# Optimization experiments

Measured on AMD Instinct MI355X. Metric: run time of the kernel, lower is better.

## Reference

```python
import jax, jax.numpy as jnp
import numpy as np

EMBED_DIM = 1024
NUM_HEADS = 16
HEAD_DIM = EMBED_DIM // NUM_HEADS


def setup_inputs() -> dict:
    key = jax.random.key(0)
    ks = jax.random.split(key, 9)
    s = 1.0 / np.sqrt(EMBED_DIM)
    mk = lambda k: jax.random.uniform(k, (EMBED_DIM, EMBED_DIM), jnp.float32, -s, s)
    bk = lambda k: jax.random.uniform(k, (EMBED_DIM,), jnp.float32, -s, s)
    return {
        "input_tensor": jax.random.normal(ks[0], (4, 2048, EMBED_DIM), jnp.float32),
        "wq": mk(ks[1]), "bq": bk(ks[2]),
        "wk": mk(ks[3]), "bk_": bk(ks[4]),
        "wv": mk(ks[5]), "bv": bk(ks[6]),
        "wo": mk(ks[7]), "bo": bk(ks[8]),
    }


def reference(input_tensor, wq, bq, wk, bk_, wv, bv, wo, bo):
    B, S, E = input_tensor.shape
    H, D = NUM_HEADS, HEAD_DIM
    # torch Linear: y = x @ W.T + b
    q = input_tensor @ wq.T + bq
    k = input_tensor @ wk.T + bk_
    v = input_tensor @ wv.T + bv
    q = q.reshape(B, S, H, D).transpose(0, 2, 1, 3)  # [B,H,S,D]
    k = k.reshape(B, S, H, D).transpose(0, 2, 1, 3)
    v = v.reshape(B, S, H, D).transpose(0, 2, 1, 3)
    scores = jnp.einsum('bhsd,bhtd->bhst', q, k) / jnp.sqrt(jnp.float32(D))
    attn = jax.nn.softmax(scores, axis=-1)  # dropout p=0 -> identity
    out = jnp.einsum('bhst,bhtd->bhsd', attn, v)
    out = out.transpose(0, 2, 1, 3).reshape(B, S, E)
    return out @ wo.T + bo
```

## Files before the change

### kernel.cpp

```cpp
#include <hip/hip_runtime.h>

typedef __bf16 bf16x8 __attribute__((ext_vector_type(8)));
typedef float  f32x4  __attribute__((ext_vector_type(4)));
typedef float  f32x16 __attribute__((ext_vector_type(16)));
typedef unsigned u32x4 __attribute__((ext_vector_type(4)));

#define NB 4
#define SEQ 2048
#define EMB 1024
#define NH 16
#define HD 64
#define MTOT (NB * SEQ)

__device__ __forceinline__ unsigned short f2bf(float f) {
    unsigned u = __float_as_uint(f);
    return (unsigned short)((u + 0x7fffu + ((u >> 16) & 1u)) >> 16);
}

__device__ __forceinline__ void gload16(const void* g, void* l) {
    __builtin_amdgcn_global_load_lds(
        (const __attribute__((address_space(1))) unsigned int*)g,
        (__attribute__((address_space(3))) unsigned int*)l,
        16, 0, 0);
}

__global__ __launch_bounds__(256) void cast_f32_bf16(
    const float* __restrict__ src, unsigned short* __restrict__ dst, int n4) {
    int i = blockIdx.x * 256 + threadIdx.x;
    if (i < n4) {
        float4 v = ((const float4*)src)[i];
        ushort4 r;
        r.x = f2bf(v.x); r.y = f2bf(v.y); r.z = f2bf(v.z); r.w = f2bf(v.w);
        ((ushort4*)dst)[i] = r;
    }
}

__global__ __launch_bounds__(256) void cast4_f32_bf16(
    const float* __restrict__ a, const float* __restrict__ b,
    const float* __restrict__ c, const float* __restrict__ d,
    unsigned short* __restrict__ oa, unsigned short* __restrict__ ob,
    unsigned short* __restrict__ oc, unsigned short* __restrict__ od) {
    int which = blockIdx.x >> 10;
    int i = (blockIdx.x & 1023) * 256 + threadIdx.x;
    const float* src = which == 0 ? a : which == 1 ? b : which == 2 ? c : d;
    unsigned short* dst = which == 0 ? oa : which == 1 ? ob : which == 2 ? oc : od;
    float4 v = ((const float4*)src)[i];
    ushort4 r;
    r.x = f2bf(v.x); r.y = f2bf(v.y); r.z = f2bf(v.z); r.w = f2bf(v.w);
    ((ushort4*)dst)[i] = r;
}

template <int MODE>
__global__ __launch_bounds__(256) void gemm_bt(
    const unsigned short* __restrict__ A, const unsigned short* __restrict__ W,
    const float* __restrict__ bias, void* __restrict__ out, float oscale) {
    constexpr int K = EMB;
    __shared__ __align__(16) unsigned short As[128 * 64];
    __shared__ __align__(16) unsigned short Bs[128 * 64];

    const int lane = threadIdx.x & 63;
    const int wv   = threadIdx.x >> 6;
    const int wr   = wv >> 1, wc = wv & 1;
    const int m0   = blockIdx.y * 128, n0 = blockIdx.x * 128;

    f32x4 acc[4][4];
#pragma unroll
    for (int a = 0; a < 4; ++a)
#pragma unroll
        for (int b = 0; b < 4; ++b) acc[a][b] = (f32x4){0.f, 0.f, 0.f, 0.f};

    for (int kt = 0; kt < K / 64; ++kt) {
        if (kt) __syncthreads();
#pragma unroll
        for (int j = 0; j < 4; ++j) {
            int rb = (wv * 4 + j) * 8;
            int r  = rb + (lane >> 3);
            int c  = (lane & 7) * 8;
            gload16(A + (size_t)(m0 + r) * K + kt * 64 + c, &As[rb * 64]);
            gload16(W + (size_t)(n0 + r) * K + kt * 64 + c, &Bs[rb * 64]);
        }
        __syncthreads();
#pragma unroll
        for (int ks = 0; ks < 2; ++ks) {
            bf16x8 af[4], bf_[4];
#pragma unroll
            for (int x = 0; x < 4; ++x) {
                af[x]  = *(const bf16x8*)&As[(wr * 64 + x * 16 + (lane & 15)) * 64 + ks * 32 + (lane >> 4) * 8];
                bf_[x] = *(const bf16x8*)&Bs[(wc * 64 + x * 16 + (lane & 15)) * 64 + ks * 32 + (lane >> 4) * 8];
            }
#pragma unroll
            for (int mi = 0; mi < 4; ++mi)
#pragma unroll
                for (int ni = 0; ni < 4; ++ni)
                    acc[mi][ni] = __builtin_amdgcn_mfma_f32_16x16x32_bf16(
                        af[mi], bf_[ni], acc[mi][ni], 0, 0, 0);
        }
    }

#pragma unroll
    for (int mi = 0; mi < 4; ++mi) {
#pragma unroll
        for (int ni = 0; ni < 4; ++ni) {
            int n = n0 + wc * 64 + ni * 16 + (lane & 15);
            float bv = bias[n];
#pragma unroll
            for (int i = 0; i < 4; ++i) {
                int m = m0 + wr * 64 + mi * 16 + (lane >> 4) * 4 + i;
                float v = (acc[mi][ni][i] + bv) * oscale;
                if (MODE == 1) {
                    ((float*)out)[(size_t)m * EMB + n] = v;
                } else {
                    int b = m >> 11, s = m & (SEQ - 1);
                    int h = n >> 6,  d = n & 63;
                    if (MODE == 0)
                        ((unsigned short*)out)[(((size_t)(b * NH + h) * SEQ + s) << 6) + d] = f2bf(v);
                    else
                        ((unsigned short*)out)[((size_t)(b * NH + h) * 64 + d) * SEQ + s] = f2bf(v);
                }
            }
        }
    }
}

__global__ __launch_bounds__(256, 4) void attn_fwd(
    const unsigned short* __restrict__ Q, const unsigned short* __restrict__ K,
    const unsigned short* __restrict__ Vt, unsigned short* __restrict__ AO) {
    const int qt = blockIdx.x;
    const int bh = blockIdx.y;
    const int lane = threadIdx.x & 63;
    const int wv   = threadIdx.x >> 6;
    const int l31  = lane & 31;
    const int lh   = lane >> 5;

    __shared__ __align__(16) unsigned short Ks[2][64 * 64];
    __shared__ __align__(16) unsigned short Vs[2][64 * 64];

    const unsigned short* Kb = K + (size_t)bh * SEQ * HD;
    const unsigned short* Vb = Vt + (size_t)bh * HD * SEQ;

    const unsigned short* Qp = Q + ((size_t)bh * SEQ + qt * 128 + wv * 32 + l31) * HD + lh * 8;
    bf16x8 qfr[4];
#pragma unroll
    for (int kc = 0; kc < 4; ++kc) qfr[kc] = *(const bf16x8*)(Qp + kc * 16);

    f32x16 oT[2];
#pragma unroll
    for (int r = 0; r < 16; ++r) { oT[0][r] = 0.f; oT[1][r] = 0.f; }
    float lacc = 0.f;

    auto stageKV = [&](int buf, int t) {
#pragma unroll
        for (int j = 0; j < 2; ++j) {
            int rb = wv * 16 + j * 8;
            int r  = rb + (lane >> 3);
            int gs = (lane & 7) ^ (r & 7);
            gload16(Kb + (size_t)(t * 64 + r) * 64 + gs * 8, &Ks[buf][rb * 64]);
            gload16(Vb + (size_t)r * SEQ + t * 64 + gs * 8, &Vs[buf][rb * 64]);
        }
    };

    stageKV(0, 0);

    for (int t = 0; t < SEQ / 64; ++t) {
        const int cur = t & 1;
        __syncthreads();
        if (t + 1 < SEQ / 64) stageKV(cur ^ 1, t + 1);

#pragma unroll
        for (int sub = 0; sub < 2; ++sub) {
            f32x16 st;
#pragma unroll
            for (int r = 0; r < 16; ++r) st[r] = 0.f;
            const int krow = sub * 32 + l31;
            __builtin_amdgcn_s_setprio(1);
#pragma unroll
            for (int kc = 0; kc < 4; ++kc) {
                int slot = (kc * 2 + lh) ^ (krow & 7);
                bf16x8 kf = *(const bf16x8*)&Ks[cur][krow * 64 + slot * 8];
                st = __builtin_amdgcn_mfma_f32_32x32x16_bf16(kf, qfr[kc], st, 0, 0, 0);
            }
            __builtin_amdgcn_s_setprio(0);

            unsigned w0, w1, w2, w3, w4, w5, w6, w7;
#define EXPPK(WI, RA, RB)                                                     \
            {                                                                 \
                float pa = __builtin_amdgcn_exp2f(st[RA]);                    \
                float pb = __builtin_amdgcn_exp2f(st[RB]);                    \
                lacc += pa + pb;                                              \
                asm("v_cvt_pk_bf16_f32 %0, %1, %2" : "=v"(WI) : "v"(pa), "v"(pb)); \
            }
            EXPPK(w0, 0, 1)  EXPPK(w1, 2, 3)  EXPPK(w2, 4, 5)  EXPPK(w3, 6, 7)
            EXPPK(w4, 8, 9)  EXPPK(w5, 10, 11) EXPPK(w6, 12, 13) EXPPK(w7, 14, 15)
#undef EXPPK
            asm volatile("v_permlane32_swap_b32 %0, %1" : "+v"(w0), "+v"(w2));
            asm volatile("v_permlane32_swap_b32 %0, %1" : "+v"(w1), "+v"(w3));
            asm volatile("v_permlane32_swap_b32 %0, %1" : "+v"(w4), "+v"(w6));
            asm volatile("v_permlane32_swap_b32 %0, %1" : "+v"(w5), "+v"(w7));
            u32x4 a0 = {w0, w1, w2, w3};
            u32x4 a1 = {w4, w5, w6, w7};
            bf16x8 pf0 = __builtin_bit_cast(bf16x8, a0);
            bf16x8 pf1 = __builtin_bit_cast(bf16x8, a1);

            __builtin_amdgcn_s_setprio(1);
#pragma unroll
            for (int dt = 0; dt < 2; ++dt) {
                int d = dt * 32 + l31;
#pragma unroll
                for (int ks = 0; ks < 2; ++ks) {
                    int slot = (sub * 4 + ks * 2 + lh) ^ (d & 7);
                    bf16x8 vf = *(const bf16x8*)&Vs[cur][d * 64 + slot * 8];
                    oT[dt] = __builtin_amdgcn_mfma_f32_32x32x16_bf16(
                        vf, ks ? pf1 : pf0, oT[dt], 0, 0, 0);
                }
            }
            __builtin_amdgcn_s_setprio(0);
        }
    }

    float l = lacc + __shfl_xor(lacc, 32);
    float inv = 1.0f / l;
    const int b = bh >> 4, h = bh & 15;
    const int q = qt * 128 + wv * 32 + l31;
    unsigned short* aor = AO + (((size_t)b * SEQ + q) * NH + h) * HD;
#pragma unroll
    for (int dt = 0; dt < 2; ++dt) {
#pragma unroll
        for (int g = 0; g < 4; ++g) {
            ushort4 o;
            o.x = f2bf(oT[dt][g * 4 + 0] * inv);
            o.y = f2bf(oT[dt][g * 4 + 1] * inv);
            o.z = f2bf(oT[dt][g * 4 + 2] * inv);
            o.w = f2bf(oT[dt][g * 4 + 3] * inv);
            *(ushort4*)(aor + dt * 32 + g * 8 + lh * 4) = o;
        }
    }
}

extern "C" void kernel_launch(void* const* d_in, const int* in_sizes, int n_in,
                              void* d_out, int out_size, void* d_ws, size_t ws_size,
                              hipStream_t stream) {
    const float* X  = (const float*)d_in[0];
    const float* wq = (const float*)d_in[1];
    const float* bq = (const float*)d_in[2];
    const float* wk = (const float*)d_in[3];
    const float* bk = (const float*)d_in[4];
    const float* wv = (const float*)d_in[5];
    const float* bv = (const float*)d_in[6];
    const float* wo = (const float*)d_in[7];
    const float* bo = (const float*)d_in[8];
    float* out = (float*)d_out;

    unsigned short* ws = (unsigned short*)d_ws;
    const size_t XE = (size_t)MTOT * EMB;
    const size_t WE = (size_t)EMB * EMB;
    unsigned short* Xb  = ws;
    unsigned short* Wqb = ws + XE;
    unsigned short* Wkb = Wqb + WE;
    unsigned short* Wvb = Wkb + WE;
    unsigned short* Wob = Wvb + WE;
    unsigned short* Qb  = Wob + WE;
    unsigned short* Kb  = Qb + XE;
    unsigned short* Vtb = Kb + XE;
    unsigned short* AOb = Xb;

    cast_f32_bf16<<<(int)(XE / 4 / 256), 256, 0, stream>>>(X, Xb, (int)(XE / 4));
    cast4_f32_bf16<<<4096, 256, 0, stream>>>(wq, wk, wv, wo, Wqb, Wkb, Wvb, Wob);

    const float CEXP = 0.18033688011112043f;
    dim3 g(EMB / 128, MTOT / 128);
    gemm_bt<0><<<g, 256, 0, stream>>>(Xb, Wqb, bq, Qb, CEXP);
    gemm_bt<0><<<g, 256, 0, stream>>>(Xb, Wkb, bk, Kb, 1.0f);
    gemm_bt<2><<<g, 256, 0, stream>>>(Xb, Wvb, bv, Vtb, 1.0f);

    attn_fwd<<<dim3(16, NB * NH), 256, 0, stream>>>(Qb, Kb, Vtb, AOb);

    gemm_bt<1><<<g, 256, 0, stream>>>(AOb, Wob, bo, out, 1.0f);
}
```

Baseline: 209.3 us.

## Fuse QKV projections into one GEMM launch and widen attention blocks to 512 threads

The three separate Q/K/V projection GEMMs become a single launch over a 3072-wide output. It relies on Wq, Wk and Wv being contiguous in the workspace so W3 indexes them as one matrix, and picks the bias, scale and output layout per 1024-column slice. The attention kernel now uses 512 threads (8 waves) covering 256 queries per block, so each staged K/V tile is shared by twice as many queries and each thread issues half as many staging loads. This cuts launch count and K/V reloads, at the cost of fewer, larger attention blocks and higher per-CU register and occupancy pressure.

```diff
diff --git a/kernel.cpp b/kernel.cpp
--- a/kernel.cpp
+++ b/kernel.cpp
@@ -50,10 +50,84 @@
     ((ushort4*)dst)[i] = r;
 }
 
-template <int MODE>
-__global__ __launch_bounds__(256) void gemm_bt(
+__global__ __launch_bounds__(256) void gemm_qkv(
+    const unsigned short* __restrict__ A, const unsigned short* __restrict__ W3,
+    const float* __restrict__ bq, const float* __restrict__ bk,
+    const float* __restrict__ bv, unsigned short* __restrict__ Qo,
+    unsigned short* __restrict__ Ko, unsigned short* __restrict__ Vto) {
+    constexpr int K = EMB;
+    __shared__ __align__(16) unsigned short As[128 * 64];
+    __shared__ __align__(16) unsigned short Bs[128 * 64];
+
+    const int lane = threadIdx.x & 63;
+    const int wv   = threadIdx.x >> 6;
+    const int wr   = wv >> 1, wc = wv & 1;
+    const int m0   = blockIdx.y * 128, n0 = blockIdx.x * 128;
+    const int proj = n0 >> 10;
+    const float* bp = proj == 0 ? bq : proj == 1 ? bk : bv;
+    const float oscale = proj == 0 ? 0.18033688011112043f : 1.0f;
+
+    f32x4 acc[4][4];
+#pragma unroll
+    for (int a = 0; a < 4; ++a)
+#pragma unroll
+        for (int b = 0; b < 4; ++b) acc[a][b] = (f32x4){0.f, 0.f, 0.f, 0.f};
+
+    for (int kt = 0; kt < K / 64; ++kt) {
+        if (kt) __syncthreads();
+#pragma unroll
+        for (int j = 0; j < 4; ++j) {
+            int rb = (wv * 4 + j) * 8;
+            int r  = rb + (lane >> 3);
+            int c  = (lane & 7) * 8;
+            gload16(A + (size_t)(m0 + r) * K + kt * 64 + c, &As[rb * 64]);
+            gload16(W3 + (size_t)(n0 + r) * K + kt * 64 + c, &Bs[rb * 64]);
+        }
+        __syncthreads();
+#pragma unroll
+        for (int ks = 0; ks < 2; ++ks) {
+            bf16x8 af[4], bf_[4];
+#pragma unroll
+            for (int x = 0; x < 4; ++x) {
+                af[x]  = *(const bf16x8*)&As[(wr * 64 + x * 16 + (lane & 15)) * 64 + ks * 32 + (lane >> 4) * 8];
+                bf_[x] = *(const bf16x8*)&Bs[(wc * 64 + x * 16 + (lane & 15)) * 64 + ks * 32 + (lane >> 4) * 8];
+            }
+#pragma unroll
+            for (int mi = 0; mi < 4; ++mi)
+#pragma unroll
+                for (int ni = 0; ni < 4; ++ni)
+                    acc[mi][ni] = __builtin_amdgcn_mfma_f32_16x16x32_bf16(
+                        af[mi], bf_[ni], acc[mi][ni], 0, 0, 0);
+        }
+    }
+
+#pragma unroll
+    for (int mi = 0; mi < 4; ++mi) {
+#pragma unroll
+        for (int ni = 0; ni < 4; ++ni) {
+            int n    = n0 + wc * 64 + ni * 16 + (lane & 15);
+            int nloc = n & 1023;
+            float bvv = bp[nloc];
+            int h = nloc >> 6, d = nloc & 63;
+#pragma unroll
+            for (int i = 0; i < 4; ++i) {
+                int m = m0 + wr * 64 + mi * 16 + (lane >> 4) * 4 + i;
+                float v = (acc[mi][ni][i] + bvv) * oscale;
+                int b = m >> 11, s = m & (SEQ - 1);
+                if (proj == 0)
+                    Qo[(((size_t)(b * NH + h) * SEQ + s) << 6) + d] = f2bf(v);
+                else if (proj == 1)
+                    Ko[(((size_t)(b * NH + h) * SEQ + s) << 6) + d] = f2bf(v);
+                else
+                    Vto[((size_t)(b * NH + h) * 64 + d) * SEQ + s] = f2bf(v);
+            }
+        }
+    }
+}
+
+__global__ __launch_bounds__(256) void gemm_out(
     const unsigned short* __restrict__ A, const unsigned short* __restrict__ W,
-    const float* __restrict__ bias, void* __restrict__ out, float oscale) {
+    const float* __restrict__ bias, float* __restrict__ out) {
     constexpr int K = EMB;
     __shared__ __align__(16) unsigned short As[128 * 64];
     __shared__ __align__(16) unsigned short Bs[128 * 64];
@@ -106,23 +180,13 @@
 #pragma unroll
             for (int i = 0; i < 4; ++i) {
                 int m = m0 + wr * 64 + mi * 16 + (lane >> 4) * 4 + i;
-                float v = (acc[mi][ni][i] + bv) * oscale;
-                if (MODE == 1) {
-                    ((float*)out)[(size_t)m * EMB + n] = v;
-                } else {
-                    int b = m >> 11, s = m & (SEQ - 1);
-                    int h = n >> 6,  d = n & 63;
-                    if (MODE == 0)
-                        ((unsigned short*)out)[(((size_t)(b * NH + h) * SEQ + s) << 6) + d] = f2bf(v);
-                    else
-                        ((unsigned short*)out)[((size_t)(b * NH + h) * 64 + d) * SEQ + s] = f2bf(v);
-                }
-            }
-        }
-    }
-}
-
-__global__ __launch_bounds__(256, 4) void attn_fwd(
+                out[(size_t)m * EMB + n] = acc[mi][ni][i] + bv;
+            }
+        }
+    }
+}
+
+__global__ __launch_bounds__(512, 4) void attn_fwd(
     const unsigned short* __restrict__ Q, const unsigned short* __restrict__ K,
     const unsigned short* __restrict__ Vt, unsigned short* __restrict__ AO) {
     const int qt = blockIdx.x;
@@ -138,7 +202,7 @@
     const unsigned short* Kb = K + (size_t)bh * SEQ * HD;
     const unsigned short* Vb = Vt + (size_t)bh * HD * SEQ;
 
-    const unsigned short* Qp = Q + ((size_t)bh * SEQ + qt * 128 + wv * 32 + l31) * HD + lh * 8;
+    const unsigned short* Qp = Q + ((size_t)bh * SEQ + qt * 256 + wv * 32 + l31) * HD + lh * 8;
     bf16x8 qfr[4];
 #pragma unroll
     for (int kc = 0; kc < 4; ++kc) qfr[kc] = *(const bf16x8*)(Qp + kc * 16);
@@ -149,14 +213,10 @@
     float lacc = 0.f;
 
     auto stageKV = [&](int buf, int t) {
-#pragma unroll
-        for (int j = 0; j < 2; ++j) {
-            int rb = wv * 16 + j * 8;
-            int r  = rb + (lane >> 3);
-            int gs = (lane & 7) ^ (r & 7);
-            gload16(Kb + (size_t)(t * 64 + r) * 64 + gs * 8, &Ks[buf][rb * 64]);
-            gload16(Vb + (size_t)r * SEQ + t * 64 + gs * 8, &Vs[buf][rb * 64]);
-        }
+        int r  = wv * 8 + (lane >> 3);
+        int gs = (lane & 7) ^ (r & 7);
+        gload16(Kb + (size_t)(t * 64 + r) * 64 + gs * 8, &Ks[buf][wv * 8 * 64]);
+        gload16(Vb + (size_t)r * SEQ + t * 64 + gs * 8, &Vs[buf][wv * 8 * 64]);
     };
 
     stageKV(0, 0);
@@ -220,7 +280,7 @@
     float l = lacc + __shfl_xor(lacc, 32);
     float inv = 1.0f / l;
     const int b = bh >> 4, h = bh & 15;
-    const int q = qt * 128 + wv * 32 + l31;
+    const int q = qt * 256 + wv * 32 + l31;
     unsigned short* aor = AO + (((size_t)b * SEQ + q) * NH + h) * HD;
 #pragma unroll
     for (int dt = 0; dt < 2; ++dt) {
@@ -266,13 +326,10 @@
     cast_f32_bf16<<<(int)(XE / 4 / 256), 256, 0, stream>>>(X, Xb, (int)(XE / 4));
     cast4_f32_bf16<<<4096, 256, 0, stream>>>(wq, wk, wv, wo, Wqb, Wkb, Wvb, Wob);
 
-    const float CEXP = 0.18033688011112043f;
-    dim3 g(EMB / 128, MTOT / 128);
-    gemm_bt<0><<<g, 256, 0, stream>>>(Xb, Wqb, bq, Qb, CEXP);
-    gemm_bt<0><<<g, 256, 0, stream>>>(Xb, Wkb, bk, Kb, 1.0f);
-    gemm_bt<2><<<g, 256, 0, stream>>>(Xb, Wvb, bv, Vtb, 1.0f);
-
-    attn_fwd<<<dim3(16, NB * NH), 256, 0, stream>>>(Qb, Kb, Vtb, AOb);
-
-    gemm_bt<1><<<g, 256, 0, stream>>>(AOb, Wob, bo, out, 1.0f);
-}
+    gemm_qkv<<<dim3(3 * EMB / 128, MTOT / 128), 256, 0, stream>>>(
+        Xb, Wqb, bq, bk, bv, Qb, Kb, Vtb);
+
+    attn_fwd<<<dim3(SEQ / 256, NB * NH), 512, 0, stream>>>(Qb, Kb, Vtb, AOb);
+
+    gemm_out<<<dim3(EMB / 128, MTOT / 128), 256, 0, stream>>>(AOb, Wob, bo, out);
+}
```

After: 202.9 us. -3.1%, faster.
